# Kernel tuning notes

Measured on AMD Instinct MI355X. Metric: run time of the kernel, lower is better.

## Reference

```python
import jax, jax.numpy as jnp
import numpy as np

B, S, D_MODEL = 2, 2048, 512
KEY_DIM, VALUE_DIM, OUTPUT_DIM, NUM_HEADS = 256, 256, 512, 8


def setup_inputs() -> dict:
    key = jax.random.key(0)
    ks = jax.random.split(key, 12)
    s = 0.02
    return {
        "V": jax.random.normal(ks[0], (B, S, D_MODEL), jnp.float32),
        "Q": jax.random.normal(ks[1], (B, S, D_MODEL), jnp.float32),
        "K": jax.random.normal(ks[2], (B, S, D_MODEL), jnp.float32),
        "mask": jax.random.normal(ks[3], (B, 1, S, S), jnp.float32),
        "Wq": jax.random.normal(ks[4], (D_MODEL, KEY_DIM), jnp.float32) * s,
        "bq": jnp.zeros((KEY_DIM,), jnp.float32),
        "Wk": jax.random.normal(ks[5], (D_MODEL, KEY_DIM), jnp.float32) * s,
        "bk": jnp.zeros((KEY_DIM,), jnp.float32),
        "Wv": jax.random.normal(ks[6], (D_MODEL, VALUE_DIM), jnp.float32) * s,
        "bv": jnp.zeros((VALUE_DIM,), jnp.float32),
        "Wo": jax.random.normal(ks[7], (VALUE_DIM, OUTPUT_DIM), jnp.float32) * s,
        "bo": jnp.zeros((OUTPUT_DIM,), jnp.float32),
    }


def _split_heads(x, num_heads):
    # [B, S, H*d] -> [B, H, S, d]
    b, s, hd = x.shape
    return x.reshape(b, s, num_heads, hd // num_heads).transpose(0, 2, 1, 3)


def reference(V, Q, K, mask, Wq, bq, Wk, bk, Wv, bv, Wo, bo):
    denom = jnp.sqrt(jnp.float32(KEY_DIM))  # NOTE: full key_dim, as in source
    q = _split_heads(Q @ Wq + bq, NUM_HEADS)  # [B,H,S,dk]
    k = _split_heads(K @ Wk + bk, NUM_HEADS)
    scores = jnp.einsum("bhqd,bhkd->bhqk", q, k) / denom
    scores = scores + mask  # soft (additive) mask
    weights = jax.nn.softmax(scores, axis=-1)
    v = _split_heads(V @ Wv + bv, NUM_HEADS)  # [B,H,S,dv]
    ctx = jnp.einsum("bhqk,bhkd->bhqd", weights, v)  # [B,H,S,dv]
    b, h, s, d = ctx.shape
    ctx = ctx.transpose(0, 2, 1, 3).reshape(b, s, h * d)  # merge heads
    return ctx @ Wo + bo
```

## Files before the change

kernel.cpp:

```cpp
#include <hip/hip_runtime.h>

typedef __attribute__((ext_vector_type(8))) short bf16x8;
typedef __attribute__((ext_vector_type(4))) float f32x4;

#define B_  2
#define S_  2048
#define DM  512
#define KD  256
#define HD  32
#define NH  8

__device__ __forceinline__ float bf2f(ushort u) {
    return __uint_as_float(((uint)u) << 16);
}
__device__ __forceinline__ ushort f2bf(float f) {
    uint x = __float_as_uint(f);
    return (ushort)((x + 0x7fffu + ((x >> 16) & 1u)) >> 16);
}
__device__ __forceinline__ uint cvt_pk_bf16(float lo, float hi) {
    uint r;
    asm("v_cvt_pk_bf16_f32 %0, %1, %2" : "=v"(r) : "v"(lo), "v"(hi));
    return r;
}
#define MFMA __builtin_amdgcn_mfma_f32_16x16x32_bf16

__device__ __forceinline__ int detect_isbf(const ushort* __restrict__ q)
{
    int lane = threadIdx.x & 63;
    int e = (q[lane] >> 7) & 0xFF;
    unsigned long long m = __ballot(e >= 100 && e <= 133);
    return __popcll(m) >= 58;
}

__global__ __launch_bounds__(256) void transpose_w(
    const void* __restrict__ Wq, const void* __restrict__ Wk, const void* __restrict__ Wv,
    const void* __restrict__ Wo,
    const void* __restrict__ bq, const void* __restrict__ bk,
    const void* __restrict__ bv, const void* __restrict__ bo,
    const ushort* __restrict__ qsrc,
    ushort* __restrict__ Wt, ushort* __restrict__ Wot, float* __restrict__ biasf)
{
    int isbf = detect_isbf(qsrc);
    int bid = blockIdx.x;
    if (bid >= 512) {
        for (int i = threadIdx.x; i < 1280; i += 256) {
            const void* bp; int off;
            if (i < 256)      { bp = bq; off = i; }
            else if (i < 512) { bp = bk; off = i - 256; }
            else if (i < 768) { bp = bv; off = i - 512; }
            else              { bp = bo; off = i - 768; }
            biasf[i] = isbf ? bf2f(((const ushort*)bp)[off]) : ((const float*)bp)[off];
        }
        return;
    }
    const void* W; int R, C; ushort* T;
    int m = bid >> 7, tix = bid & 127;
    if (m < 3) { W = (m == 0) ? Wq : (m == 1) ? Wk : Wv; R = 512; C = 256; T = Wt + m * 131072; }
    else       { W = Wo; R = 256; C = 512; T = Wot; }
    int tilesPerRow = C >> 5;
    int r0 = (tix / tilesPerRow) * 32, c0 = (tix % tilesPerRow) * 32;
    __shared__ float lds[32][33];
    int t = threadIdx.x;
    int rr = t >> 3, cc = (t & 7) * 4;
    if (isbf) {
        const ushort* Ws = (const ushort*)W;
        #pragma unroll
        for (int j = 0; j < 4; ++j) lds[rr][cc + j] = bf2f(Ws[(size_t)(r0 + rr) * C + c0 + cc + j]);
    } else {
        float4 v = *(const float4*)((const float*)W + (size_t)(r0 + rr) * C + c0 + cc);
        lds[rr][cc + 0] = v.x; lds[rr][cc + 1] = v.y; lds[rr][cc + 2] = v.z; lds[rr][cc + 3] = v.w;
    }
    __syncthreads();
    ushort4 o;
    o.x = f2bf(lds[cc + 0][rr]); o.y = f2bf(lds[cc + 1][rr]);
    o.z = f2bf(lds[cc + 2][rr]); o.w = f2bf(lds[cc + 3][rr]);
    int n = c0 + rr, k = r0 + cc;
    *(ushort4*)(T + ((((size_t)(n >> 4) * (R >> 3) + (k >> 3)) * 16 + (n & 15)) << 3) + (k & 7)) = o;
}

__global__ __launch_bounds__(256) void qkv_gemm(
    const void* __restrict__ Q, const void* __restrict__ K, const void* __restrict__ V,
    const ushort* __restrict__ Wt, const float* __restrict__ biasf,
    ushort* __restrict__ qh, ushort* __restrict__ kh, ushort* __restrict__ vT)
{
    int isbf = detect_isbf((const ushort*)Q);
    int y = blockIdx.y;
    const void* X = (y == 0) ? Q : (y == 1) ? K : V;
    int wave = threadIdx.x >> 6, lane = threadIdx.x & 63;
    int l16 = lane & 15, quad = lane >> 4;
    int m0 = blockIdx.x * 16;
    int n0 = wave * 64;
    const ushort* W = Wt + (size_t)y * (256 * 512);

    auto loadA = [&](int ks, bf16x8* a) {
        if (isbf) {
            *a = *(const bf16x8*)((const ushort*)X + (size_t)(m0 + l16) * 512 + ks + quad * 8);
        } else {
            const float* p = (const float*)X + (size_t)(m0 + l16) * 512 + ks + quad * 8;
            float4 f0 = *(const float4*)p, f1 = *(const float4*)(p + 4);
            union { uint u[4]; bf16x8 v; } cv;
            cv.u[0] = cvt_pk_bf16(f0.x, f0.y);
            cv.u[1] = cvt_pk_bf16(f0.z, f0.w);
            cv.u[2] = cvt_pk_bf16(f1.x, f1.y);
            cv.u[3] = cvt_pk_bf16(f1.z, f1.w);
            *a = cv.v;
        }
    };
    auto loadB = [&](int ks, bf16x8* b) {
        #pragma unroll
        for (int j = 0; j < 4; ++j)
            b[j] = *(const bf16x8*)(W + (((size_t)((n0 >> 4) + j) * 64 + (ks >> 3) + quad) * 16 + l16) * 8);
    };

    f32x4 acc[4] = {};
    bf16x8 aC, bC[4], aN, bN[4];
    loadA(0, &aC); loadB(0, bC);
    for (int ks = 0; ks < 512; ks += 32) {
        if (ks + 32 < 512) { loadA(ks + 32, &aN); loadB(ks + 32, bN); }
        #pragma unroll
        for (int j = 0; j < 4; ++j)
            acc[j] = MFMA(aC, bC[j], acc[j], 0, 0, 0);
        aC = aN;
        #pragma unroll
        for (int j = 0; j < 4; ++j) bC[j] = bN[j];
    }
    if (y < 2) {
        ushort* out = (y == 0) ? qh : kh;
        #pragma unroll
        for (int j = 0; j < 4; ++j) {
            int n = n0 + 16 * j + l16;
            float bs = biasf[y * 256 + n];
            int h = n >> 5, d = n & 31;
            #pragma unroll
            for (int r = 0; r < 4; ++r) {
                int rg = m0 + quad * 4 + r;
                int bb = rg >> 11, ss = rg & 2047;
                out[((((size_t)bb * NH + h) * S_ + ss) << 5) + d] = f2bf(acc[j][r] + bs);
            }
        }
    } else {
        int rg0 = m0 + quad * 4;
        int bb = rg0 >> 11, s0 = rg0 & 2047;
        #pragma unroll
        for (int j = 0; j < 4; ++j) {
            int n = n0 + 16 * j + l16;
            float bs = biasf[2 * 256 + n];
            int h = n >> 5, d = n & 31;
            ushort4 o;
            o.x = f2bf(acc[j][0] + bs); o.y = f2bf(acc[j][1] + bs);
            o.z = f2bf(acc[j][2] + bs); o.w = f2bf(acc[j][3] + bs);
            *(ushort4*)(vT + (((size_t)(bb * NH + h) * HD + d) * S_) + s0) = o;
        }
    }
}

__global__ __launch_bounds__(256) void attn(
    const ushort* __restrict__ qh, const ushort* __restrict__ kh,
    const ushort* __restrict__ vT, const void* __restrict__ maskp,
    float* __restrict__ pO, float* __restrict__ pl)
{
    __shared__ __align__(16) ushort ldsP[4][2][16][72];
    int isbf;
    {
        int lane = threadIdx.x & 63;
        ushort u = ((const ushort*)maskp)[lane];
        int e = (u >> 7) & 0xFF;
        unsigned long long m = __ballot(e >= 100 && e <= 133);
        isbf = __popcll(m) >= 58;
    }
    int wave = threadIdx.x >> 6, lane = threadIdx.x & 63;
    int l16 = lane & 15, quad = lane >> 4;
    int wid = blockIdx.x * 4 + wave;
    int chunk = wid & 1, qt32 = (wid >> 1) & 63, bh = wid >> 7;
    int b = bh >> 3;
    int q0 = qt32 * 32;
    const ushort* qb = qh + (size_t)bh * S_ * HD;
    const ushort* kb = kh + (size_t)bh * S_ * HD;
    const ushort* vb = vT + (size_t)bh * HD * S_;
    const ushort* mbb = (const ushort*)maskp + (size_t)b * S_ * S_;
    const float*  mbf = (const float*)maskp  + (size_t)b * S_ * S_;
    size_t mbase = (size_t)(q0 + quad * 4) * S_ + l16;

    bf16x8 aq0 = *(const bf16x8*)(qb + (size_t)(q0 + l16) * HD + quad * 8);
    bf16x8 aq1 = *(const bf16x8*)(qb + (size_t)(q0 + 16 + l16) * HD + quad * 8);
    f32x4 O00 = {0,0,0,0}, O01 = {0,0,0,0}, O10 = {0,0,0,0}, O11 = {0,0,0,0};
    const f32x4 zero = {0, 0, 0, 0};
    float lsum0[4] = {0,0,0,0}, lsum1[4] = {0,0,0,0};
    float M0[16], M1[16];
    bf16x8 Vf[4];

    auto loadK = [&](int k0, bf16x8* Kf) {
        #pragma unroll
        for (int c = 0; c < 4; ++c)
            Kf[c] = *(const bf16x8*)(kb + (size_t)(k0 + c * 16 + l16) * HD + quad * 8);
    };
    auto loadM = [&](int k0) {
        if (isbf) {
            #pragma unroll
            for (int r = 0; r < 4; ++r) {
                const ushort* p = mbb + mbase + (size_t)r * S_ + k0;
                #pragma unroll
                for (int c = 0; c < 4; ++c) M0[c * 4 + r] = bf2f(p[c * 16]);
                p += (size_t)16 * S_;
                #pragma unroll
                for (int c = 0; c < 4; ++c) M1[c * 4 + r] = bf2f(p[c * 16]);
            }
        } else {
            #pragma unroll
            for (int r = 0; r < 4; ++r) {
                const float* p = mbf + mbase + (size_t)r * S_ + k0;
                #pragma unroll
                for (int c = 0; c < 4; ++c) M0[c * 4 + r] = p[c * 16];
                p += (size_t)16 * S_;
                #pragma unroll
                for (int c = 0; c < 4; ++c) M1[c * 4 + r] = p[c * 16];
            }
        }
    };
    auto loadV = [&](int k0) {
        Vf[0] = *(const bf16x8*)(vb + (size_t)l16 * S_ + k0 + quad * 8);
        Vf[1] = *(const bf16x8*)(vb + (size_t)l16 * S_ + k0 + 32 + quad * 8);
        Vf[2] = *(const bf16x8*)(vb + (size_t)(16 + l16) * S_ + k0 + quad * 8);
        Vf[3] = *(const bf16x8*)(vb + (size_t)(16 + l16) * S_ + k0 + 32 + quad * 8);
    };

    auto substep = [&](bf16x8* Kcur, int nextk0, bf16x8* Knext) {
        if (nextk0 >= 0) loadK(nextk0, Knext);
        f32x4 Sc0[4], Sc1[4];
        #pragma unroll
        for (int c = 0; c < 4; ++c) Sc0[c] = MFMA(aq0, Kcur[c], zero, 0, 0, 0);
        #pragma unroll
        for (int c = 0; c < 4; ++c) Sc1[c] = MFMA(aq1, Kcur[c], zero, 0, 0, 0);
        #pragma unroll
        for (int c = 0; c < 4; ++c) {
            float p0v[4], p1v[4];
            #pragma unroll
            for (int r = 0; r < 4; ++r) {
                float p = __expf(fmaf(Sc0[c][r], 0.0625f, M0[c * 4 + r]));
                lsum0[r] += p; p0v[r] = p;
                float q = __expf(fmaf(Sc1[c][r], 0.0625f, M1[c * 4 + r]));
                lsum1[r] += q; p1v[r] = q;
            }
            #pragma unroll
            for (int r = 0; r < 4; r += 2) {
                uint w0 = cvt_pk_bf16(p0v[r], p0v[r + 1]);
                ldsP[wave][0][quad * 4 + r][c * 16 + l16]     = (ushort)w0;
                ldsP[wave][0][quad * 4 + r + 1][c * 16 + l16] = (ushort)(w0 >> 16);
                uint w1 = cvt_pk_bf16(p1v[r], p1v[r + 1]);
                ldsP[wave][1][quad * 4 + r][c * 16 + l16]     = (ushort)w1;
                ldsP[wave][1][quad * 4 + r + 1][c * 16 + l16] = (ushort)(w1 >> 16);
            }
        }
        if (nextk0 >= 0) loadM(nextk0);
        asm volatile("s_waitcnt lgkmcnt(0)" ::: "memory");
        bf16x8 aP00 = *(const bf16x8*)&ldsP[wave][0][l16][quad * 8];
        bf16x8 aP01 = *(const bf16x8*)&ldsP[wave][0][l16][32 + quad * 8];
        bf16x8 aP10 = *(const bf16x8*)&ldsP[wave][1][l16][quad * 8];
        bf16x8 aP11 = *(const bf16x8*)&ldsP[wave][1][l16][32 + quad * 8];
        O00 = MFMA(aP00, Vf[0], O00, 0, 0, 0);
        O00 = MFMA(aP01, Vf[1], O00, 0, 0, 0);
        O01 = MFMA(aP00, Vf[2], O01, 0, 0, 0);
        O01 = MFMA(aP01, Vf[3], O01, 0, 0, 0);
        O10 = MFMA(aP10, Vf[0], O10, 0, 0, 0);
        O10 = MFMA(aP11, Vf[1], O10, 0, 0, 0);
        O11 = MFMA(aP10, Vf[2], O11, 0, 0, 0);
        O11 = MFMA(aP11, Vf[3], O11, 0, 0, 0);
        if (nextk0 >= 0) loadV(nextk0);
    };

    int kbase = chunk * 1024;
    bf16x8 Ka[4], Kb2[4];
    loadK(kbase, Ka); loadM(kbase); loadV(kbase);
    for (int t = 0; t < 16; t += 2) {
        substep(Ka, kbase + (t + 1) * 64, Kb2);
        substep(Kb2, (t + 2 < 16) ? kbase + (t + 2) * 64 : -1, Ka);
    }

    #pragma unroll
    for (int tile = 0; tile < 2; ++tile) {
        int wid16 = ((bh * 128) + (qt32 * 2 + tile)) * 2 + chunk;
        float* po = pO + (size_t)wid16 * 512;
        f32x4 Oa = tile ? O10 : O00, Ob = tile ? O11 : O01;
        float* ls = tile ? lsum1 : lsum0;
        #pragma unroll
        for (int r = 0; r < 4; ++r) {
            int row = quad * 4 + r;
            po[row * 32 + l16]      = Oa[r];
            po[row * 32 + 16 + l16] = Ob[r];
            float sthis = ls[r];
            #pragma unroll
            for (int off = 8; off; off >>= 1) sthis += __shfl_xor(sthis, off, 16);
            if (l16 == 0) pl[wid16 * 16 + row] = sthis;
        }
    }
}

__global__ __launch_bounds__(256) void out_proj(
    const float* __restrict__ pO, const float* __restrict__ pl,
    const ushort* __restrict__ Wot, const float* __restrict__ biasf,
    float* __restrict__ out)
{
    int wave = threadIdx.x >> 6, lane = threadIdx.x & 63;
    int l16 = lane & 15, quad = lane >> 4;
    int m0 = (blockIdx.x >> 1) * 16;
    int n0 = (blockIdx.x & 1) * 256 + wave * 64;
    f32x4 acc[4] = {};
    for (int ks = 0; ks < 256; ks += 32) {
        int h = ks >> 5;
        bf16x8 a, b[4];
        {
            int row = m0 + l16;
            int bb = row >> 11, s = row & 2047;
            int qt = s >> 4, r16 = s & 15;
            int wid0 = ((bb * NH + h) << 8) | (qt << 1);
            const float* p0 = pO + (size_t)wid0 * 512 + r16 * 32 + quad * 8;
            float4 x0 = *(const float4*)p0,         x1 = *(const float4*)(p0 + 4);
            float4 y0 = *(const float4*)(p0 + 512), y1 = *(const float4*)(p0 + 516);
            float il = 1.0f / (pl[wid0 * 16 + r16] + pl[(wid0 + 1) * 16 + r16]);
            union { uint u[4]; bf16x8 v; } cv;
            cv.u[0] = cvt_pk_bf16((x0.x + y0.x) * il, (x0.y + y0.y) * il);
            cv.u[1] = cvt_pk_bf16((x0.z + y0.z) * il, (x0.w + y0.w) * il);
            cv.u[2] = cvt_pk_bf16((x1.x + y1.x) * il, (x1.y + y1.y) * il);
            cv.u[3] = cvt_pk_bf16((x1.z + y1.z) * il, (x1.w + y1.w) * il);
            a = cv.v;
        }
        #pragma unroll
        for (int j = 0; j < 4; ++j)
            b[j] = *(const bf16x8*)(Wot + (((size_t)((n0 >> 4) + j) * 32 + (ks >> 3) + quad) * 16 + l16) * 8);
        #pragma unroll
        for (int j = 0; j < 4; ++j)
            acc[j] = MFMA(a, b[j], acc[j], 0, 0, 0);
    }
    #pragma unroll
    for (int j = 0; j < 4; ++j) {
        int n = n0 + 16 * j + l16;
        float bs = biasf[768 + n];
        #pragma unroll
        for (int r = 0; r < 4; ++r) {
            int rg = m0 + quad * 4 + r;
            out[(size_t)rg * DM + n] = acc[j][r] + bs;
        }
    }
}

extern "C" void kernel_launch(void* const* d_in, const int* in_sizes, int n_in,
                              void* d_out, int out_size, void* d_ws, size_t ws_size,
                              hipStream_t stream)
{
    const void* V    = d_in[0];
    const void* Q    = d_in[1];
    const void* K    = d_in[2];
    const void* mask = d_in[3];
    const void* Wq = d_in[4];  const void* bq = d_in[5];
    const void* Wk = d_in[6];  const void* bk = d_in[7];
    const void* Wv = d_in[8];  const void* bv = d_in[9];
    const void* Wo = d_in[10]; const void* bo = d_in[11];
    float* out = (float*)d_out;

    char* ws = (char*)d_ws;
    float*  biasf = (float*)ws;
    ushort* Wt  = (ushort*)(ws + 8192);
    ushort* Wot = Wt  + 393216;
    ushort* qh  = Wot + 131072;
    ushort* kh  = qh  + 1048576;
    ushort* vT  = kh  + 1048576;
    float*  pO  = (float*)(vT + 1048576);
    float*  pl  = pO + 4096 * 512;

    transpose_w<<<513, 256, 0, stream>>>(Wq, Wk, Wv, Wo, bq, bk, bv, bo,
                                         (const ushort*)Q, Wt, Wot, biasf);
    qkv_gemm<<<dim3(256, 3), 256, 0, stream>>>(Q, K, V, Wt, biasf, qh, kh, vT);
    attn<<<512, 256, 0, stream>>>(qh, kh, vT, mask, pO, pl);
    out_proj<<<512, 256, 0, stream>>>(pO, pl, Wot, biasf, out);
}
```

Before: 172.9 us.

## Switch attention to 32x32x16 MFMA with register-resident P via permlane swap

Rewrites the attention inner loop to use 32x32x16 bf16 MFMA, computing S^T = K·Q^T so each lane holds a query column. The softmax probabilities are repacked into the PV operand with v_permlane32_swap instead of a round trip through LDS. The mask is now loaded with coalesced float4 reads and staged through a padded, double-buffered LDS tile rather than read as scattered scalars, and the key step shrinks to 32. This trades LDS traffic for P against LDS traffic for the mask, and adds more loop iterations and more register pressure.

Result: slower. 183.3 us (+6.1%).

```diff
diff --git a/kernel.cpp b/kernel.cpp
--- a/kernel.cpp
+++ b/kernel.cpp
@@ -2,6 +2,7 @@
 
 typedef __attribute__((ext_vector_type(8))) short bf16x8;
 typedef __attribute__((ext_vector_type(4))) float f32x4;
+typedef __attribute__((ext_vector_type(16))) float f32x16;
 
 #define B_  2
 #define S_  2048
@@ -23,6 +24,7 @@
     return r;
 }
 #define MFMA __builtin_amdgcn_mfma_f32_16x16x32_bf16
+#define MFMA32 __builtin_amdgcn_mfma_f32_32x32x16_bf16
 
 __device__ __forceinline__ int detect_isbf(const ushort* __restrict__ q)
 {
@@ -159,7 +161,7 @@
     const ushort* __restrict__ vT, const void* __restrict__ maskp,
     float* __restrict__ pO, float* __restrict__ pl)
 {
-    __shared__ __align__(16) ushort ldsP[4][2][16][72];
+    __shared__ float ldsM[4][2][32][33];
     int isbf;
     {
         int lane = threadIdx.x & 63;
@@ -169,7 +171,7 @@
         isbf = __popcll(m) >= 58;
     }
     int wave = threadIdx.x >> 6, lane = threadIdx.x & 63;
-    int l16 = lane & 15, quad = lane >> 4;
+    int l31 = lane & 31, hi = lane >> 5;
     int wid = blockIdx.x * 4 + wave;
     int chunk = wid & 1, qt32 = (wid >> 1) & 63, bh = wid >> 7;
     int b = bh >> 3;
@@ -179,119 +181,108 @@
     const ushort* vb = vT + (size_t)bh * HD * S_;
     const ushort* mbb = (const ushort*)maskp + (size_t)b * S_ * S_;
     const float*  mbf = (const float*)maskp  + (size_t)b * S_ * S_;
-    size_t mbase = (size_t)(q0 + quad * 4) * S_ + l16;
-
-    bf16x8 aq0 = *(const bf16x8*)(qb + (size_t)(q0 + l16) * HD + quad * 8);
-    bf16x8 aq1 = *(const bf16x8*)(qb + (size_t)(q0 + 16 + l16) * HD + quad * 8);
-    f32x4 O00 = {0,0,0,0}, O01 = {0,0,0,0}, O10 = {0,0,0,0}, O11 = {0,0,0,0};
-    const f32x4 zero = {0, 0, 0, 0};
-    float lsum0[4] = {0,0,0,0}, lsum1[4] = {0,0,0,0};
-    float M0[16], M1[16];
-    bf16x8 Vf[4];
-
-    auto loadK = [&](int k0, bf16x8* Kf) {
-        #pragma unroll
-        for (int c = 0; c < 4; ++c)
-            Kf[c] = *(const bf16x8*)(kb + (size_t)(k0 + c * 16 + l16) * HD + quad * 8);
-    };
-    auto loadM = [&](int k0) {
+
+    bf16x8 bq0 = *(const bf16x8*)(qb + (size_t)(q0 + l31) * HD + hi * 8);
+    bf16x8 bq1 = *(const bf16x8*)(qb + (size_t)(q0 + l31) * HD + 16 + hi * 8);
+
+    f32x16 O = {0,0,0,0,0,0,0,0,0,0,0,0,0,0,0,0};
+    const f32x16 Z = {0,0,0,0,0,0,0,0,0,0,0,0,0,0,0,0};
+    float lsum = 0.0f;
+
+    int srow = (lane >> 3) & 7, scol = (lane & 7) * 4;
+    float4 g[4];
+
+    auto loadMg = [&](int k0) {
         if (isbf) {
             #pragma unroll
-            for (int r = 0; r < 4; ++r) {
-                const ushort* p = mbb + mbase + (size_t)r * S_ + k0;
-                #pragma unroll
-                for (int c = 0; c < 4; ++c) M0[c * 4 + r] = bf2f(p[c * 16]);
-                p += (size_t)16 * S_;
-                #pragma unroll
-                for (int c = 0; c < 4; ++c) M1[c * 4 + r] = bf2f(p[c * 16]);
+            for (int i = 0; i < 4; ++i) {
+                ushort4 u = *(const ushort4*)(mbb + (size_t)(q0 + i * 8 + srow) * S_ + k0 + scol);
+                float4 f; f.x = bf2f(u.x); f.y = bf2f(u.y); f.z = bf2f(u.z); f.w = bf2f(u.w);
+                g[i] = f;
             }
         } else {
             #pragma unroll
-            for (int r = 0; r < 4; ++r) {
-                const float* p = mbf + mbase + (size_t)r * S_ + k0;
-                #pragma unroll
-                for (int c = 0; c < 4; ++c) M0[c * 4 + r] = p[c * 16];
-                p += (size_t)16 * S_;
-                #pragma unroll
-                for (int c = 0; c < 4; ++c) M1[c * 4 + r] = p[c * 16];
-            }
-        }
-    };
-    auto loadV = [&](int k0) {
-        Vf[0] = *(const bf16x8*)(vb + (size_t)l16 * S_ + k0 + quad * 8);
-        Vf[1] = *(const bf16x8*)(vb + (size_t)l16 * S_ + k0 + 32 + quad * 8);
-        Vf[2] = *(const bf16x8*)(vb + (size_t)(16 + l16) * S_ + k0 + quad * 8);
-        Vf[3] = *(const bf16x8*)(vb + (size_t)(16 + l16) * S_ + k0 + 32 + quad * 8);
-    };
-
-    auto substep = [&](bf16x8* Kcur, int nextk0, bf16x8* Knext) {
-        if (nextk0 >= 0) loadK(nextk0, Knext);
-        f32x4 Sc0[4], Sc1[4];
-        #pragma unroll
-        for (int c = 0; c < 4; ++c) Sc0[c] = MFMA(aq0, Kcur[c], zero, 0, 0, 0);
-        #pragma unroll
-        for (int c = 0; c < 4; ++c) Sc1[c] = MFMA(aq1, Kcur[c], zero, 0, 0, 0);
-        #pragma unroll
-        for (int c = 0; c < 4; ++c) {
-            float p0v[4], p1v[4];
-            #pragma unroll
-            for (int r = 0; r < 4; ++r) {
-                float p = __expf(fmaf(Sc0[c][r], 0.0625f, M0[c * 4 + r]));
-                lsum0[r] += p; p0v[r] = p;
-                float q = __expf(fmaf(Sc1[c][r], 0.0625f, M1[c * 4 + r]));
-                lsum1[r] += q; p1v[r] = q;
-            }
-            #pragma unroll
-            for (int r = 0; r < 4; r += 2) {
-                uint w0 = cvt_pk_bf16(p0v[r], p0v[r + 1]);
-                ldsP[wave][0][quad * 4 + r][c * 16 + l16]     = (ushort)w0;
-                ldsP[wave][0][quad * 4 + r + 1][c * 16 + l16] = (ushort)(w0 >> 16);
-                uint w1 = cvt_pk_bf16(p1v[r], p1v[r + 1]);
-                ldsP[wave][1][quad * 4 + r][c * 16 + l16]     = (ushort)w1;
-                ldsP[wave][1][quad * 4 + r + 1][c * 16 + l16] = (ushort)(w1 >> 16);
-            }
-        }
-        if (nextk0 >= 0) loadM(nextk0);
-        asm volatile("s_waitcnt lgkmcnt(0)" ::: "memory");
-        bf16x8 aP00 = *(const bf16x8*)&ldsP[wave][0][l16][quad * 8];
-        bf16x8 aP01 = *(const bf16x8*)&ldsP[wave][0][l16][32 + quad * 8];
-        bf16x8 aP10 = *(const bf16x8*)&ldsP[wave][1][l16][quad * 8];
-        bf16x8 aP11 = *(const bf16x8*)&ldsP[wave][1][l16][32 + quad * 8];
-        O00 = MFMA(aP00, Vf[0], O00, 0, 0, 0);
-        O00 = MFMA(aP01, Vf[1], O00, 0, 0, 0);
-        O01 = MFMA(aP00, Vf[2], O01, 0, 0, 0);
-        O01 = MFMA(aP01, Vf[3], O01, 0, 0, 0);
-        O10 = MFMA(aP10, Vf[0], O10, 0, 0, 0);
-        O10 = MFMA(aP11, Vf[1], O10, 0, 0, 0);
-        O11 = MFMA(aP10, Vf[2], O11, 0, 0, 0);
-        O11 = MFMA(aP11, Vf[3], O11, 0, 0, 0);
-        if (nextk0 >= 0) loadV(nextk0);
+            for (int i = 0; i < 4; ++i)
+                g[i] = *(const float4*)(mbf + (size_t)(q0 + i * 8 + srow) * S_ + k0 + scol);
+        }
+    };
+    auto writeM = [&](int buf) {
+        #pragma unroll
+        for (int i = 0; i < 4; ++i) {
+            ldsM[wave][buf][i * 8 + srow][scol + 0] = g[i].x;
+            ldsM[wave][buf][i * 8 + srow][scol + 1] = g[i].y;
+            ldsM[wave][buf][i * 8 + srow][scol + 2] = g[i].z;
+            ldsM[wave][buf][i * 8 + srow][scol + 3] = g[i].w;
+        }
+    };
+    auto loadK = [&](int k0, bf16x8* K2) {
+        K2[0] = *(const bf16x8*)(kb + (size_t)(k0 + l31) * HD + hi * 8);
+        K2[1] = *(const bf16x8*)(kb + (size_t)(k0 + l31) * HD + 16 + hi * 8);
+    };
+    auto loadV = [&](int k0, bf16x8* V2) {
+        V2[0] = *(const bf16x8*)(vb + (size_t)l31 * S_ + k0 + hi * 8);
+        V2[1] = *(const bf16x8*)(vb + (size_t)l31 * S_ + k0 + 16 + hi * 8);
     };
 
     int kbase = chunk * 1024;
-    bf16x8 Ka[4], Kb2[4];
-    loadK(kbase, Ka); loadM(kbase); loadV(kbase);
-    for (int t = 0; t < 16; t += 2) {
-        substep(Ka, kbase + (t + 1) * 64, Kb2);
-        substep(Kb2, (t + 2 < 16) ? kbase + (t + 2) * 64 : -1, Ka);
-    }
-
+
+    auto sub = [&](int buf, bf16x8* Kc, bf16x8* Vc, bf16x8* Kn, bf16x8* Vn, int t) {
+        float Mreg[16];
+        #pragma unroll
+        for (int r = 0; r < 16; ++r)
+            Mreg[r] = ldsM[wave][buf][l31][(r & 3) + ((r >> 2) << 3) + (hi << 2)];
+        int ktn = kbase + ((t + 1 < 32) ? (t + 1) : 31) * 32;
+        loadK(ktn, Kn); loadV(ktn, Vn);
+        f32x16 S = MFMA32(Kc[0], bq0, Z, 0, 0, 0);
+        S = MFMA32(Kc[1], bq1, S, 0, 0, 0);
+        writeM(buf ^ 1);
+        int ktn2 = kbase + ((t + 2 < 32) ? (t + 2) : 31) * 32;
+        loadMg(ktn2);
+        float p[16];
+        #pragma unroll
+        for (int r = 0; r < 16; ++r) {
+            p[r] = __expf(fmaf(S[r], 0.0625f, Mreg[r]));
+            lsum += p[r];
+        }
+        union { uint u[4]; bf16x8 v; } pa0, pa1;
+        {
+            uint u0 = cvt_pk_bf16(p[0], p[1]),  w0 = cvt_pk_bf16(p[4], p[5]);
+            uint u1 = cvt_pk_bf16(p[2], p[3]),  w1 = cvt_pk_bf16(p[6], p[7]);
+            asm volatile("v_permlane32_swap_b32 %0, %1" : "+v"(u0), "+v"(w0));
+            asm volatile("v_permlane32_swap_b32 %0, %1" : "+v"(u1), "+v"(w1));
+            pa0.u[0] = u0; pa0.u[1] = u1; pa0.u[2] = w0; pa0.u[3] = w1;
+            uint u2 = cvt_pk_bf16(p[8], p[9]),   w2 = cvt_pk_bf16(p[12], p[13]);
+            uint u3 = cvt_pk_bf16(p[10], p[11]), w3 = cvt_pk_bf16(p[14], p[15]);
+            asm volatile("v_permlane32_swap_b32 %0, %1" : "+v"(u2), "+v"(w2));
+            asm volatile("v_permlane32_swap_b32 %0, %1" : "+v"(u3), "+v"(w3));
+            pa1.u[0] = u2; pa1.u[1] = u3; pa1.u[2] = w2; pa1.u[3] = w3;
+        }
+        O = MFMA32(pa0.v, Vc[0], O, 0, 0, 0);
+        O = MFMA32(pa1.v, Vc[1], O, 0, 0, 0);
+    };
+
+    bf16x8 KA[2], VA[2], KB[2], VB[2];
+    loadK(kbase, KA); loadV(kbase, VA);
+    loadMg(kbase); writeM(0);
+    loadMg(kbase + 32);
+    for (int t = 0; t < 32; t += 2) {
+        sub(0, KA, VA, KB, VB, t);
+        sub(1, KB, VB, KA, VA, t + 1);
+    }
+
+    float tot = lsum + __shfl_xor(lsum, 32, 64);
+    int wid16_0 = ((bh * 128) + qt32 * 2 + 0) * 2 + chunk;
+    int wid16_1 = ((bh * 128) + qt32 * 2 + 1) * 2 + chunk;
+    if (lane < 32) {
+        int q = l31;
+        int w16 = (q < 16) ? wid16_0 : wid16_1;
+        pl[w16 * 16 + (q & 15)] = tot;
+    }
     #pragma unroll
-    for (int tile = 0; tile < 2; ++tile) {
-        int wid16 = ((bh * 128) + (qt32 * 2 + tile)) * 2 + chunk;
-        float* po = pO + (size_t)wid16 * 512;
-        f32x4 Oa = tile ? O10 : O00, Ob = tile ? O11 : O01;
-        float* ls = tile ? lsum1 : lsum0;
-        #pragma unroll
-        for (int r = 0; r < 4; ++r) {
-            int row = quad * 4 + r;
-            po[row * 32 + l16]      = Oa[r];
-            po[row * 32 + 16 + l16] = Ob[r];
-            float sthis = ls[r];
-            #pragma unroll
-            for (int off = 8; off; off >>= 1) sthis += __shfl_xor(sthis, off, 16);
-            if (l16 == 0) pl[wid16 * 16 + row] = sthis;
-        }
+    for (int r = 0; r < 16; ++r) {
+        int q = (r & 3) + ((r >> 2) << 3) + (hi << 2);
+        int w16 = (q < 16) ? wid16_0 : wid16_1;
+        pO[(size_t)w16 * 512 + (q & 15) * 32 + l31] = O[r];
     }
 }
 
```
